# Performance work log

Measured on AMD Instinct MI355X. Metric: run time of the kernel, lower is better.

The kernel has to match this reference:

```python
import jax, jax.numpy as jnp
import numpy as np

# Config (matches init_kwargs)
B, L, D = 2, 2048, 1024
QH, KVH, HD, FFN = 8, 2, 128, 4096
EPS = 1.1920929e-07  # torch RMSNorm default eps = finfo(float32).eps


def _rope_ts():
    d2 = HD // 2
    freq_exp = (2.0 / HD) * jnp.arange(d2, dtype=jnp.float32)
    return 10000.0 ** freq_exp  # [d2]


def _rope(x):
    # x: [B, L, H, HD], rotated in fp32 (matches x.float() in source)
    d2 = HD // 2
    pos = jnp.arange(L, dtype=jnp.float32)
    rad = pos[:, None] / _rope_ts()[None, :]          # [L, d2]
    s = jnp.sin(rad)[None, :, None, :]                # [1, L, 1, d2]
    c = jnp.cos(rad)[None, :, None, :]
    xf = x.astype(jnp.float32)
    x1, x2 = xf[..., :d2], xf[..., d2:]
    return jnp.concatenate([x1 * c - x2 * s, x2 * c + x1 * s], axis=-1).astype(x.dtype)


def _rmsnorm(x, w):
    xf = x.astype(jnp.float32)
    r = jax.lax.rsqrt(jnp.mean(xf * xf, axis=-1, keepdims=True) + EPS)
    return (xf * r).astype(x.dtype) * w


def setup_inputs() -> dict:
    key = jax.random.key(0)
    ks = jax.random.split(key, 9)
    s = 0.02
    return {
        "x": jax.random.normal(ks[0], (B, L, D), dtype=jnp.float32),
        "ln1_w": jnp.ones((D,), dtype=jnp.float32),
        "wq": jax.random.normal(ks[1], (D, QH * HD), dtype=jnp.float32) * s,
        "wk": jax.random.normal(ks[2], (D, KVH * HD), dtype=jnp.float32) * s,
        "wv": jax.random.normal(ks[3], (D, KVH * HD), dtype=jnp.float32) * s,
        "wo": jax.random.normal(ks[4], (QH * HD, D), dtype=jnp.float32) * s,
        "ln2_w": jnp.ones((D,), dtype=jnp.float32),
        "wg": jax.random.normal(ks[5], (D, FFN), dtype=jnp.float32) * s,
        "wu": jax.random.normal(ks[6], (D, FFN), dtype=jnp.float32) * s,
        "wd": jax.random.normal(ks[7], (FFN, D), dtype=jnp.float32) * s,
    }


def reference(x, ln1_w, wq, wk, wv, wo, ln2_w, wg, wu, wd):
    residual = x
    h = _rmsnorm(x, ln1_w)

    q = _rope((h @ wq).reshape(B, L, QH, HD))          # [B,L,QH,HD]
    k = _rope((h @ wk).reshape(B, L, KVH, HD))         # [B,L,KVH,HD]
    v = (h @ wv).reshape(B, L, KVH, HD)

    rep = QH // KVH  # kv_map = floor(arange(QH)*KVH/QH) == repeat each kv head `rep` times
    qh = jnp.transpose(q, (0, 2, 1, 3)).astype(jnp.float32)                       # [B,QH,L,HD]
    kh = jnp.transpose(jnp.repeat(k, rep, axis=2), (0, 2, 1, 3)).astype(jnp.float32)
    vh = jnp.transpose(jnp.repeat(v, rep, axis=2), (0, 2, 1, 3)).astype(jnp.float32)

    scores = jnp.einsum("bhqd,bhkd->bhqk", qh, kh) / jnp.sqrt(jnp.float32(HD))    # [B,QH,L,L]
    causal = jnp.triu(jnp.ones((L, L), dtype=bool), 1)
    scores = jnp.where(causal, -jnp.inf, scores)
    attn = jax.nn.softmax(scores, axis=-1)
    ctx = jnp.einsum("bhqk,bhkd->bhqd", attn, vh)                                 # [B,QH,L,HD]
    ctx = jnp.transpose(ctx, (0, 2, 1, 3)).reshape(B, L, QH * HD).astype(x.dtype)

    x = ctx @ wo + residual
    residual = x
    h = _rmsnorm(x, ln2_w)
    return (jax.nn.silu(h @ wg) * (h @ wu)) @ wd + residual
```

## Files before the change

kernel.cpp:

```cpp
#include <hip/hip_runtime.h>
#include <hip/hip_bf16.h>
#include <math.h>

#define B_ 2
#define L_ 2048
#define D_ 1024
#define QH_ 8
#define KVH_ 2
#define HD_ 128
#define FFN_ 4096
#define T_ (B_ * L_)
#define EPS_ 1.1920929e-07f

typedef __bf16 bf16x8 __attribute__((ext_vector_type(8)));
typedef float floatx4 __attribute__((ext_vector_type(4)));
typedef unsigned short ushortx8 __attribute__((ext_vector_type(8)));

__device__ __forceinline__ unsigned short f2bf(float f) {
  union { float f; unsigned int u; } v;
  v.f = f;
  unsigned int r = v.u + 0x7FFFu + ((v.u >> 16) & 1u);
  return (unsigned short)(r >> 16);
}
__device__ __forceinline__ float bf2f(unsigned short u) {
  union { unsigned int u; float f; } v;
  v.u = ((unsigned int)u) << 16;
  return v.f;
}
__device__ __forceinline__ void gload_lds16(const void* g, void* l) {
  __builtin_amdgcn_global_load_lds((const __attribute__((address_space(1))) void*)g,
                                   (__attribute__((address_space(3))) void*)l, 16, 0, 0);
}

__global__ __launch_bounds__(256) void transpose_cast(const float* __restrict__ in,
                                                      unsigned short* __restrict__ out,
                                                      int K, int N) {
  __shared__ float tile[32][33];
  int n0 = blockIdx.x * 32, k0 = blockIdx.y * 32;
  int tx = threadIdx.x & 31, ty = threadIdx.x >> 5;
  for (int r = ty; r < 32; r += 8) tile[r][tx] = in[(size_t)(k0 + r) * N + n0 + tx];
  __syncthreads();
  for (int r = ty; r < 32; r += 8)
    out[(size_t)(n0 + r) * K + k0 + tx] = f2bf(tile[tx][r]);
}

__global__ __launch_bounds__(256) void rmsnorm_bf16_kernel(const float* __restrict__ x,
                                                           const float* __restrict__ w,
                                                           unsigned short* __restrict__ o) {
  int row = blockIdx.x;
  int t = threadIdx.x;
  const float* xr = x + (size_t)row * D_;
  float4 xv = *(const float4*)(xr + t * 4);
  float ss = xv.x * xv.x + xv.y * xv.y + xv.z * xv.z + xv.w * xv.w;
#pragma unroll
  for (int off = 32; off >= 1; off >>= 1) ss += __shfl_xor(ss, off);
  __shared__ float red[4];
  if ((t & 63) == 0) red[t >> 6] = ss;
  __syncthreads();
  float total = red[0] + red[1] + red[2] + red[3];
  float r = rsqrtf(total * (1.0f / (float)D_) + EPS_);
  float4 wv = *(const float4*)(w + t * 4);
  unsigned short* op = o + (size_t)row * D_ + t * 4;
  op[0] = f2bf(xv.x * r * wv.x);
  op[1] = f2bf(xv.y * r * wv.y);
  op[2] = f2bf(xv.z * r * wv.z);
  op[3] = f2bf(xv.w * r * wv.w);
}

template <int EPI, int MW>
__global__ __launch_bounds__(256) void gemm_bf16(const unsigned short* __restrict__ A,
                                                 const unsigned short* __restrict__ BT,
                                                 const float* __restrict__ R,
                                                 float* __restrict__ C,
                                                 int M, int N, int K) {
  constexpr int AI = MW / 16;
  __shared__ unsigned short As[2 * MW * 32];
  __shared__ unsigned short Bs[128 * 32];
  int t = threadIdx.x;
  int lane = t & 63, wave = t >> 6;
  int m0 = blockIdx.y * (2 * MW), n0 = blockIdx.x * 128;

  int row_a = t >> 2, kc = (t & 3) * 8;
  const unsigned short* ga0 = A + (size_t)(m0 + row_a) * K + kc;
  const unsigned short* ga1 = A + (size_t)(m0 + 64 + row_a) * K + kc;
  const unsigned short* gb0 = BT + (size_t)(n0 + row_a) * K + kc;
  const unsigned short* gb1 = BT + (size_t)(n0 + 64 + row_a) * K + kc;
  unsigned short* lA0 = As + wave * 512;
  unsigned short* lA1 = As + 2048 + wave * 512;
  unsigned short* lB0 = Bs + wave * 512;
  unsigned short* lB1 = Bs + 2048 + wave * 512;

  int wm = (wave & 1) * MW, wn = (wave >> 1) * 64;
  int fr = lane & 15, quad = lane >> 4;
  const unsigned short* arp = As + (size_t)(wm + fr) * 32 + quad * 8;
  const unsigned short* brp = Bs + (size_t)(wn + fr) * 32 + quad * 8;

  floatx4 acc[AI][4];
#pragma unroll
  for (int i = 0; i < AI; i++)
#pragma unroll
    for (int j = 0; j < 4; j++) acc[i][j] = (floatx4){0.f, 0.f, 0.f, 0.f};

  for (int k0 = 0; k0 < K; k0 += 32) {
    gload_lds16(ga0 + k0, lA0);
    if (MW == 64) gload_lds16(ga1 + k0, lA1);
    gload_lds16(gb0 + k0, lB0);
    gload_lds16(gb1 + k0, lB1);
    __syncthreads();
    bf16x8 af[AI], bfr[4];
#pragma unroll
    for (int i = 0; i < AI; i++)
      af[i] = __builtin_bit_cast(bf16x8, *(const ushortx8*)(arp + i * 16 * 32));
#pragma unroll
    for (int j = 0; j < 4; j++)
      bfr[j] = __builtin_bit_cast(bf16x8, *(const ushortx8*)(brp + j * 16 * 32));
#pragma unroll
    for (int i = 0; i < AI; i++)
#pragma unroll
      for (int j = 0; j < 4; j++)
        acc[i][j] = __builtin_amdgcn_mfma_f32_16x16x32_bf16(af[i], bfr[j], acc[i][j], 0, 0, 0);
    __syncthreads();
  }

  int orow = m0 + wm + quad * 4;
  int ocol = n0 + wn + fr;
#pragma unroll
  for (int i = 0; i < AI; i++) {
#pragma unroll
    for (int r = 0; r < 4; r++) {
      int row = orow + i * 16 + r;
#pragma unroll
      for (int j = 0; j < 4; j++) {
        size_t idx = (size_t)row * N + ocol + j * 16;
        float v = acc[i][j][r];
        if (EPI == 0) C[idx] = v;
        else C[idx] = v + R[idx];
      }
    }
  }
}

__global__ __launch_bounds__(256, 2) void gemm_gateup(const unsigned short* __restrict__ A,
                                                      const unsigned short* __restrict__ BgT,
                                                      const unsigned short* __restrict__ BuT,
                                                      unsigned short* __restrict__ Cb,
                                                      int M, int K) {
  constexpr int N = FFN_;
  __shared__ unsigned short As[128 * 32];
  __shared__ unsigned short Bgs[128 * 32];
  __shared__ unsigned short Bus[128 * 32];
  int t = threadIdx.x;
  int lane = t & 63, wave = t >> 6;
  int m0 = blockIdx.y * 128, n0 = blockIdx.x * 128;

  int row_a = t >> 2, kc = (t & 3) * 8;
  const unsigned short* ga0 = A + (size_t)(m0 + row_a) * K + kc;
  const unsigned short* ga1 = A + (size_t)(m0 + 64 + row_a) * K + kc;
  const unsigned short* gg0 = BgT + (size_t)(n0 + row_a) * K + kc;
  const unsigned short* gg1 = BgT + (size_t)(n0 + 64 + row_a) * K + kc;
  const unsigned short* gu0 = BuT + (size_t)(n0 + row_a) * K + kc;
  const unsigned short* gu1 = BuT + (size_t)(n0 + 64 + row_a) * K + kc;
  unsigned short* lA0 = As + wave * 512;
  unsigned short* lA1 = As + 2048 + wave * 512;
  unsigned short* lG0 = Bgs + wave * 512;
  unsigned short* lG1 = Bgs + 2048 + wave * 512;
  unsigned short* lU0 = Bus + wave * 512;
  unsigned short* lU1 = Bus + 2048 + wave * 512;

  int wm = (wave & 1) * 64, wn = (wave >> 1) * 64;
  int fr = lane & 15, quad = lane >> 4;
  const unsigned short* arp = As + (size_t)(wm + fr) * 32 + quad * 8;
  const unsigned short* grp = Bgs + (size_t)(wn + fr) * 32 + quad * 8;
  const unsigned short* urp = Bus + (size_t)(wn + fr) * 32 + quad * 8;

  floatx4 accg[4][4], accu[4][4];
#pragma unroll
  for (int i = 0; i < 4; i++)
#pragma unroll
    for (int j = 0; j < 4; j++) {
      accg[i][j] = (floatx4){0.f, 0.f, 0.f, 0.f};
      accu[i][j] = (floatx4){0.f, 0.f, 0.f, 0.f};
    }

  for (int k0 = 0; k0 < K; k0 += 32) {
    gload_lds16(ga0 + k0, lA0);
    gload_lds16(ga1 + k0, lA1);
    gload_lds16(gg0 + k0, lG0);
    gload_lds16(gg1 + k0, lG1);
    gload_lds16(gu0 + k0, lU0);
    gload_lds16(gu1 + k0, lU1);
    __syncthreads();
    bf16x8 af[4], bg[4], bu[4];
#pragma unroll
    for (int i = 0; i < 4; i++) {
      af[i] = __builtin_bit_cast(bf16x8, *(const ushortx8*)(arp + i * 16 * 32));
      bg[i] = __builtin_bit_cast(bf16x8, *(const ushortx8*)(grp + i * 16 * 32));
      bu[i] = __builtin_bit_cast(bf16x8, *(const ushortx8*)(urp + i * 16 * 32));
    }
#pragma unroll
    for (int i = 0; i < 4; i++)
#pragma unroll
      for (int j = 0; j < 4; j++) {
        accg[i][j] = __builtin_amdgcn_mfma_f32_16x16x32_bf16(af[i], bg[j], accg[i][j], 0, 0, 0);
        accu[i][j] = __builtin_amdgcn_mfma_f32_16x16x32_bf16(af[i], bu[j], accu[i][j], 0, 0, 0);
      }
    __syncthreads();
  }

  int orow = m0 + wm + quad * 4;
  int ocol = n0 + wn + fr;
#pragma unroll
  for (int i = 0; i < 4; i++) {
#pragma unroll
    for (int r = 0; r < 4; r++) {
      int row = orow + i * 16 + r;
#pragma unroll
      for (int j = 0; j < 4; j++) {
        float g = accg[i][j][r];
        float u = accu[i][j][r];
        Cb[(size_t)row * N + ocol + j * 16] = f2bf(g / (1.f + __expf(-g)) * u);
      }
    }
  }
}

__global__ __launch_bounds__(256) void rope_kernel(float* __restrict__ x, int stride,
                                                   int nh_shift, int total) {
  int idx = blockIdx.x * 256 + threadIdx.x;
  if (idx >= total) return;
  int d2 = idx & 63;
  int rest = idx >> 6;
  int NH = 1 << nh_shift;
  int head = rest & (NH - 1);
  int tok = rest >> nh_shift;
  int pos = tok & (L_ - 1);
  float inv_ts = expf(-0.14391156831f * (float)d2);
  float rad = (float)pos * inv_ts;
  float s = sinf(rad), c = cosf(rad);
  float* p = x + (size_t)tok * stride + head * HD_ + d2;
  float x1 = p[0], x2 = p[64];
  p[0] = x1 * c - x2 * s;
  p[64] = x2 * c + x1 * s;
}

__global__ __launch_bounds__(256) void convert_k_rope(const float* __restrict__ qkv,
                                                      unsigned short* __restrict__ Kb) {
  int id = blockIdx.x * 256 + threadIdx.x;
  int d2 = id & 63;
  int key = (id >> 6) & (L_ - 1);
  int kvh = (id >> 17) & 1;
  int b = id >> 18;
  const float* src = qkv + (size_t)(b * L_ + key) * 1536 + 1024 + kvh * HD_ + d2;
  float x1 = src[0], x2 = src[64];
  float inv_ts = expf(-0.14391156831f * (float)d2);
  float rad = (float)key * inv_ts;
  float s = sinf(rad), c = cosf(rad);
  unsigned short* dst = Kb + ((size_t)(b * KVH_ + kvh) * L_ + key) * HD_;
  int sw = key & 15;
  dst[((d2 >> 3) ^ sw) * 8 + (d2 & 7)] = f2bf(x1 * c - x2 * s);
  dst[(((d2 >> 3) | 8) ^ sw) * 8 + (d2 & 7)] = f2bf(x2 * c + x1 * s);
}

__global__ __launch_bounds__(256) void convert_v(const float* __restrict__ qkv,
                                                 unsigned short* __restrict__ Vt) {
  __shared__ float tile[32][66];
  int key0 = blockIdx.x * 64, hd0 = blockIdx.y * 32;
  int bk = blockIdx.z;
  int b = bk >> 1, kvh = bk & 1;
  int t = threadIdx.x;
  int key_l = t >> 2, hq = t & 3;
  const float* src =
      qkv + (size_t)(b * L_ + key0 + key_l) * 1536 + 1280 + kvh * HD_ + hd0 + hq * 8;
  float4 v0 = *(const float4*)src;
  float4 v1 = *(const float4*)(src + 4);
  tile[hq * 8 + 0][key_l] = v0.x;
  tile[hq * 8 + 1][key_l] = v0.y;
  tile[hq * 8 + 2][key_l] = v0.z;
  tile[hq * 8 + 3][key_l] = v0.w;
  tile[hq * 8 + 4][key_l] = v1.x;
  tile[hq * 8 + 5][key_l] = v1.y;
  tile[hq * 8 + 6][key_l] = v1.z;
  tile[hq * 8 + 7][key_l] = v1.w;
  __syncthreads();
  int hdl = t >> 3, cp = t & 7;
  int kc = cp ^ (hdl & 7);
  ushortx8 ob;
#pragma unroll
  for (int j = 0; j < 8; j++) ob[j] = f2bf(tile[hdl][kc * 8 + j]);
  unsigned short* dst = Vt + ((size_t)bk * HD_ + hd0 + hdl) * L_ + key0 + cp * 8;
  *(ushortx8*)dst = ob;
}

__global__ __launch_bounds__(256) void attn_mfma(const float* __restrict__ qkv,
                                                 const unsigned short* __restrict__ Kb,
                                                 const unsigned short* __restrict__ Vt,
                                                 unsigned short* __restrict__ ctx) {
  __shared__ unsigned short Ks[64 * 128];
  __shared__ unsigned short Vs[128 * 64];
  __shared__ unsigned short Ps[4][16 * 72];
  const float scale = 0.08838834764831843f;
  int id = blockIdx.x;
  int bh = id & 15;
  int p_ = id >> 4;
  int qt = (p_ < 16) ? p_ : 47 - p_;
  int b = bh >> 3, h = bh & 7;
  int bk = b * KVH_ + (h >> 2);
  int q0 = qt * 64;
  int t = threadIdx.x, lane = t & 63, w = t >> 6;
  int fr = lane & 15, quad = lane >> 4;

  const float* qrow = qkv + (size_t)(b * L_ + q0 + w * 16 + fr) * 1536 + h * HD_;
  bf16x8 qf[4];
#pragma unroll
  for (int kb = 0; kb < 4; kb++) {
    float4 a = *(const float4*)(qrow + kb * 32 + quad * 8);
    float4 c = *(const float4*)(qrow + kb * 32 + quad * 8 + 4);
    qf[kb][0] = (__bf16)(a.x * scale);
    qf[kb][1] = (__bf16)(a.y * scale);
    qf[kb][2] = (__bf16)(a.z * scale);
    qf[kb][3] = (__bf16)(a.w * scale);
    qf[kb][4] = (__bf16)(c.x * scale);
    qf[kb][5] = (__bf16)(c.y * scale);
    qf[kb][6] = (__bf16)(c.z * scale);
    qf[kb][7] = (__bf16)(c.w * scale);
  }

  floatx4 o_acc[8];
#pragma unroll
  for (int nt = 0; nt < 8; nt++) o_acc[nt] = (floatx4){0.f, 0.f, 0.f, 0.f};
  float m_r[4], l_r[4];
#pragma unroll
  for (int r = 0; r < 4; r++) {
    m_r[r] = -__builtin_inff();
    l_r[r] = 0.f;
  }
  unsigned short* Psw = Ps[w];
  const unsigned short* kgb = Kb + (size_t)bk * L_ * HD_;
  const unsigned short* vgb = Vt + (size_t)bk * HD_ * L_;
  int rowg0 = q0 + w * 16 + quad * 4;

  for (int kt = 0; kt <= qt; kt++) {
    int kstart = kt * 64;
    __syncthreads();
    const unsigned short* ksrc = kgb + (size_t)kstart * HD_;
#pragma unroll
    for (int it = 0; it < 4; it++) {
      int sl = it * 4 + w;
      gload_lds16(ksrc + sl * 512 + lane * 8, Ks + sl * 512);
    }
#pragma unroll
    for (int it = 0; it < 4; it++) {
      int sl = it * 4 + w;
      gload_lds16(vgb + (size_t)(sl * 8 + (lane >> 3)) * L_ + kstart + (lane & 7) * 8,
                  Vs + sl * 512);
    }
    __syncthreads();

    floatx4 s_acc[4];
#pragma unroll
    for (int jt = 0; jt < 4; jt++) s_acc[jt] = (floatx4){0.f, 0.f, 0.f, 0.f};
#pragma unroll
    for (int kb = 0; kb < 4; kb++) {
#pragma unroll
      for (int jt = 0; jt < 4; jt++) {
        bf16x8 kf = __builtin_bit_cast(
            bf16x8, *(const ushortx8*)(Ks + (jt * 16 + fr) * 128 +
                                       (((kb * 4 + quad) ^ fr) * 8)));
        s_acc[jt] = __builtin_amdgcn_mfma_f32_16x16x32_bf16(qf[kb], kf, s_acc[jt], 0, 0, 0);
      }
    }

    float pvv[4][4];
    float alpha[4];
#pragma unroll
    for (int r = 0; r < 4; r++) {
      float mt = -__builtin_inff();
#pragma unroll
      for (int jt = 0; jt < 4; jt++) {
        int keyg = kstart + jt * 16 + fr;
        float sv = (keyg <= rowg0 + r) ? s_acc[jt][r] : -__builtin_inff();
        pvv[jt][r] = sv;
        mt = fmaxf(mt, sv);
      }
      mt = fmaxf(mt, __shfl_xor(mt, 1));
      mt = fmaxf(mt, __shfl_xor(mt, 2));
      mt = fmaxf(mt, __shfl_xor(mt, 4));
      mt = fmaxf(mt, __shfl_xor(mt, 8));
      float mn = fmaxf(m_r[r], mt);
      alpha[r] = __expf(m_r[r] - mn);
      m_r[r] = mn;
      float lt = 0.f;
#pragma unroll
      for (int jt = 0; jt < 4; jt++) {
        float pp = __expf(pvv[jt][r] - mn);
        pvv[jt][r] = pp;
        lt += pp;
      }
      lt += __shfl_xor(lt, 1);
      lt += __shfl_xor(lt, 2);
      lt += __shfl_xor(lt, 4);
      lt += __shfl_xor(lt, 8);
      l_r[r] = l_r[r] * alpha[r] + lt;
    }
#pragma unroll
    for (int nt = 0; nt < 8; nt++) {
      o_acc[nt][0] *= alpha[0];
      o_acc[nt][1] *= alpha[1];
      o_acc[nt][2] *= alpha[2];
      o_acc[nt][3] *= alpha[3];
    }
#pragma unroll
    for (int r = 0; r < 4; r++)
#pragma unroll
      for (int jt = 0; jt < 4; jt++)
        Psw[(quad * 4 + r) * 72 + jt * 16 + fr] = f2bf(pvv[jt][r]);
    bf16x8 pf0 = __builtin_bit_cast(bf16x8, *(const ushortx8*)(Psw + fr * 72 + quad * 8));
    bf16x8 pf1 =
        __builtin_bit_cast(bf16x8, *(const ushortx8*)(Psw + fr * 72 + 32 + quad * 8));
#pragma unroll
    for (int nt = 0; nt < 8; nt++) {
      bf16x8 vf0 = __builtin_bit_cast(
          bf16x8,
          *(const ushortx8*)(Vs + (nt * 16 + fr) * 64 + ((quad ^ (fr & 7)) * 8)));
      bf16x8 vf1 = __builtin_bit_cast(
          bf16x8,
          *(const ushortx8*)(Vs + (nt * 16 + fr) * 64 + (((4 + quad) ^ (fr & 7)) * 8)));
      o_acc[nt] = __builtin_amdgcn_mfma_f32_16x16x32_bf16(pf0, vf0, o_acc[nt], 0, 0, 0);
      o_acc[nt] = __builtin_amdgcn_mfma_f32_16x16x32_bf16(pf1, vf1, o_acc[nt], 0, 0, 0);
    }
  }

  unsigned short* ob =
      ctx + (size_t)(b * L_ + q0 + w * 16 + quad * 4) * 1024 + h * HD_ + fr;
#pragma unroll
  for (int r = 0; r < 4; r++) {
    float inv = 1.f / l_r[r];
    unsigned short* orow = ob + (size_t)r * 1024;
#pragma unroll
    for (int nt = 0; nt < 8; nt++) orow[nt * 16] = f2bf(o_acc[nt][r] * inv);
  }
}

extern "C" void kernel_launch(void* const* d_in, const int* in_sizes, int n_in,
                              void* d_out, int out_size, void* d_ws, size_t ws_size,
                              hipStream_t stream) {
  const float* x    = (const float*)d_in[0];
  const float* ln1w = (const float*)d_in[1];
  const float* wq   = (const float*)d_in[2];
  const float* wk   = (const float*)d_in[3];
  const float* wvp  = (const float*)d_in[4];
  const float* wo   = (const float*)d_in[5];
  const float* ln2w = (const float*)d_in[6];
  const float* wg   = (const float*)d_in[7];
  const float* wu   = (const float*)d_in[8];
  const float* wd   = (const float*)d_in[9];
  float* out = (float*)d_out;
  char* ws = (char*)d_ws;

  unsigned short* wT = (unsigned short*)ws;
  unsigned short* wqkvT = wT;
  unsigned short* woT = wT + 1572864;
  unsigned short* wgT = wT + 2621440;
  unsigned short* wuT = wT + 6815744;
  unsigned short* wdT = wT + 11010048;

  unsigned short* h_bf = (unsigned short*)(ws + 30408704);
  float* qkv = (float*)(ws + 38797312);
  float* x2 = qkv;
  unsigned short* h2_bf = (unsigned short*)(ws + 38797312 + 16777216);
  unsigned short* ctx_bf = h_bf;

  size_t gbase = 63963136;
  bool full = ws_size >= (size_t)97517568;
  unsigned short* Kb = (unsigned short*)(ws + gbase);
  unsigned short* Vt = (unsigned short*)(ws + gbase + 2097152u);
  unsigned short* gu = (unsigned short*)(ws + gbase);

  dim3 blk(256);

  transpose_cast<<<dim3(32, 32), blk, 0, stream>>>(wq, wqkvT, 1024, 1024);
  transpose_cast<<<dim3(8, 32), blk, 0, stream>>>(wk, wqkvT + 1048576, 1024, 256);
  transpose_cast<<<dim3(8, 32), blk, 0, stream>>>(wvp, wqkvT + 1310720, 1024, 256);
  transpose_cast<<<dim3(32, 32), blk, 0, stream>>>(wo, woT, 1024, 1024);
  transpose_cast<<<dim3(128, 32), blk, 0, stream>>>(wg, wgT, 1024, 4096);
  transpose_cast<<<dim3(128, 32), blk, 0, stream>>>(wu, wuT, 1024, 4096);
  transpose_cast<<<dim3(32, 128), blk, 0, stream>>>(wd, wdT, 4096, 1024);

  rmsnorm_bf16_kernel<<<T_, blk, 0, stream>>>(x, ln1w, h_bf);
  gemm_bf16<0, 32><<<dim3(12, 64), blk, 0, stream>>>(h_bf, wqkvT, nullptr, qkv,
                                                     T_, 1536, 1024);
  rope_kernel<<<(T_ * QH_ * 64) / 256, blk, 0, stream>>>(qkv, 1536, 3, T_ * QH_ * 64);
  convert_k_rope<<<(B_ * KVH_ * L_ * 64) / 256, blk, 0, stream>>>(qkv, Kb);
  convert_v<<<dim3(32, 4, 4), blk, 0, stream>>>(qkv, Vt);
  attn_mfma<<<dim3(512), blk, 0, stream>>>(qkv, Kb, Vt, ctx_bf);
  gemm_bf16<1, 32><<<dim3(8, 64), blk, 0, stream>>>(ctx_bf, woT, x, x2, T_, 1024, 1024);
  rmsnorm_bf16_kernel<<<T_, blk, 0, stream>>>(x2, ln2w, h2_bf);

  if (full) {
    gemm_gateup<<<dim3(32, 32), blk, 0, stream>>>(h2_bf, wgT, wuT, gu, T_, 1024);
    gemm_bf16<1, 32><<<dim3(8, 64), blk, 0, stream>>>(gu, wdT, x2, out, T_, 1024, FFN_);
  } else {
    for (int c = 0; c < 4; c++) {
      const unsigned short* h2c = h2_bf + (size_t)c * 1024 * 1024;
      const float* x2c = x2 + (size_t)c * 1024 * 1024;
      float* outc = out + (size_t)c * 1024 * 1024;
      gemm_gateup<<<dim3(32, 8), blk, 0, stream>>>(h2c, wgT, wuT, gu, 1024, 1024);
      gemm_bf16<1, 32><<<dim3(8, 16), blk, 0, stream>>>(gu, wdT, x2c, outc, 1024, 1024, FFN_);
    }
  }
}
```

Before: 426.7 us.

## Fuse weight prep with rmsnorm, store QKV as bf16, fuse RoPE into attention

```diff
diff --git a/kernel.cpp b/kernel.cpp
--- a/kernel.cpp
+++ b/kernel.cpp
@@ -15,6 +15,7 @@
 typedef __bf16 bf16x8 __attribute__((ext_vector_type(8)));
 typedef float floatx4 __attribute__((ext_vector_type(4)));
 typedef unsigned short ushortx8 __attribute__((ext_vector_type(8)));
+typedef unsigned short ushortx4 __attribute__((ext_vector_type(4)));
 
 __device__ __forceinline__ unsigned short f2bf(float f) {
   union { float f; unsigned int u; } v;
@@ -32,29 +33,31 @@
                                    (__attribute__((address_space(3))) void*)l, 16, 0, 0);
 }
 
-__global__ __launch_bounds__(256) void transpose_cast(const float* __restrict__ in,
-                                                      unsigned short* __restrict__ out,
-                                                      int K, int N) {
+__device__ __forceinline__ void tile_tc(const float* __restrict__ in,
+                                        unsigned short* __restrict__ out,
+                                        int K, int N, int n0, int k0) {
   __shared__ float tile[32][33];
-  int n0 = blockIdx.x * 32, k0 = blockIdx.y * 32;
-  int tx = threadIdx.x & 31, ty = threadIdx.x >> 5;
+  int t = threadIdx.x;
+  int tx = t & 31, ty = t >> 5;
   for (int r = ty; r < 32; r += 8) tile[r][tx] = in[(size_t)(k0 + r) * N + n0 + tx];
   __syncthreads();
-  for (int r = ty; r < 32; r += 8)
-    out[(size_t)(n0 + r) * K + k0 + tx] = f2bf(tile[tx][r]);
-}
-
-__global__ __launch_bounds__(256) void rmsnorm_bf16_kernel(const float* __restrict__ x,
-                                                           const float* __restrict__ w,
-                                                           unsigned short* __restrict__ o) {
-  int row = blockIdx.x;
+  int nr = t >> 3, kq = t & 7;
+  ushortx4 o4;
+#pragma unroll
+  for (int j = 0; j < 4; j++) o4[j] = f2bf(tile[kq * 4 + j][nr]);
+  *(ushortx4*)(out + (size_t)(n0 + nr) * K + k0 + kq * 4) = o4;
+}
+
+__device__ __forceinline__ void rmsnorm_row(const float* __restrict__ x,
+                                            const float* __restrict__ w,
+                                            unsigned short* __restrict__ o, int row) {
+  __shared__ float red[4];
   int t = threadIdx.x;
   const float* xr = x + (size_t)row * D_;
   float4 xv = *(const float4*)(xr + t * 4);
   float ss = xv.x * xv.x + xv.y * xv.y + xv.z * xv.z + xv.w * xv.w;
 #pragma unroll
   for (int off = 32; off >= 1; off >>= 1) ss += __shfl_xor(ss, off);
-  __shared__ float red[4];
   if ((t & 63) == 0) red[t >> 6] = ss;
   __syncthreads();
   float total = red[0] + red[1] + red[2] + red[3];
@@ -67,11 +70,44 @@
   op[3] = f2bf(xv.w * r * wv.w);
 }
 
+__global__ __launch_bounds__(256) void prep_all(
+    const float* __restrict__ wq, const float* __restrict__ wk,
+    const float* __restrict__ wv, const float* __restrict__ wo,
+    const float* __restrict__ wg, const float* __restrict__ wu,
+    const float* __restrict__ wd, unsigned short* __restrict__ wT,
+    const float* __restrict__ x, const float* __restrict__ ln1w,
+    unsigned short* __restrict__ h_bf) {
+  int bid = blockIdx.x;
+  if (bid < 14848) {
+    const float* in;
+    unsigned short* out;
+    int K, N, nt, base;
+    if (bid < 1024)       { in = wq; out = wT;            K = 1024; N = 1024; nt = 32;  base = 0; }
+    else if (bid < 1280)  { in = wk; out = wT + 1048576;  K = 1024; N = 256;  nt = 8;   base = 1024; }
+    else if (bid < 1536)  { in = wv; out = wT + 1310720;  K = 1024; N = 256;  nt = 8;   base = 1280; }
+    else if (bid < 2560)  { in = wo; out = wT + 1572864;  K = 1024; N = 1024; nt = 32;  base = 1536; }
+    else if (bid < 6656)  { in = wg; out = wT + 2621440;  K = 1024; N = 4096; nt = 128; base = 2560; }
+    else if (bid < 10752) { in = wu; out = wT + 6815744;  K = 1024; N = 4096; nt = 128; base = 6656; }
+    else                  { in = wd; out = wT + 11010048; K = 4096; N = 1024; nt = 32;  base = 10752; }
+    int idx = bid - base;
+    tile_tc(in, out, K, N, (idx % nt) * 32, (idx / nt) * 32);
+  } else {
+    rmsnorm_row(x, ln1w, h_bf, bid - 14848);
+  }
+}
+
+__global__ __launch_bounds__(256) void rmsnorm_bf16_kernel(const float* __restrict__ x,
+                                                           const float* __restrict__ w,
+                                                           unsigned short* __restrict__ o) {
+  rmsnorm_row(x, w, o, blockIdx.x);
+}
+
 template <int EPI, int MW>
 __global__ __launch_bounds__(256) void gemm_bf16(const unsigned short* __restrict__ A,
                                                  const unsigned short* __restrict__ BT,
                                                  const float* __restrict__ R,
                                                  float* __restrict__ C,
+                                                 unsigned short* __restrict__ Cb,
                                                  int M, int N, int K) {
   constexpr int AI = MW / 16;
   __shared__ unsigned short As[2 * MW * 32];
@@ -134,7 +170,9 @@
         size_t idx = (size_t)row * N + ocol + j * 16;
         float v = acc[i][j][r];
         if (EPI == 0) C[idx] = v;
-        else C[idx] = v + R[idx];
+        else if (EPI == 1) C[idx] = v + R[idx];
+        else if (EPI == 2) C[idx] = v + C[idx];
+        else Cb[idx] = f2bf(v);
       }
     }
   }
@@ -224,74 +262,50 @@
   }
 }
 
-__global__ __launch_bounds__(256) void rope_kernel(float* __restrict__ x, int stride,
-                                                   int nh_shift, int total) {
-  int idx = blockIdx.x * 256 + threadIdx.x;
-  if (idx >= total) return;
-  int d2 = idx & 63;
-  int rest = idx >> 6;
-  int NH = 1 << nh_shift;
-  int head = rest & (NH - 1);
-  int tok = rest >> nh_shift;
-  int pos = tok & (L_ - 1);
-  float inv_ts = expf(-0.14391156831f * (float)d2);
-  float rad = (float)pos * inv_ts;
-  float s = sinf(rad), c = cosf(rad);
-  float* p = x + (size_t)tok * stride + head * HD_ + d2;
-  float x1 = p[0], x2 = p[64];
-  p[0] = x1 * c - x2 * s;
-  p[64] = x2 * c + x1 * s;
-}
-
-__global__ __launch_bounds__(256) void convert_k_rope(const float* __restrict__ qkv,
-                                                      unsigned short* __restrict__ Kb) {
-  int id = blockIdx.x * 256 + threadIdx.x;
-  int d2 = id & 63;
-  int key = (id >> 6) & (L_ - 1);
-  int kvh = (id >> 17) & 1;
-  int b = id >> 18;
-  const float* src = qkv + (size_t)(b * L_ + key) * 1536 + 1024 + kvh * HD_ + d2;
-  float x1 = src[0], x2 = src[64];
-  float inv_ts = expf(-0.14391156831f * (float)d2);
-  float rad = (float)key * inv_ts;
-  float s = sinf(rad), c = cosf(rad);
-  unsigned short* dst = Kb + ((size_t)(b * KVH_ + kvh) * L_ + key) * HD_;
-  int sw = key & 15;
-  dst[((d2 >> 3) ^ sw) * 8 + (d2 & 7)] = f2bf(x1 * c - x2 * s);
-  dst[(((d2 >> 3) | 8) ^ sw) * 8 + (d2 & 7)] = f2bf(x2 * c + x1 * s);
-}
-
-__global__ __launch_bounds__(256) void convert_v(const float* __restrict__ qkv,
-                                                 unsigned short* __restrict__ Vt) {
-  __shared__ float tile[32][66];
-  int key0 = blockIdx.x * 64, hd0 = blockIdx.y * 32;
-  int bk = blockIdx.z;
-  int b = bk >> 1, kvh = bk & 1;
-  int t = threadIdx.x;
-  int key_l = t >> 2, hq = t & 3;
-  const float* src =
-      qkv + (size_t)(b * L_ + key0 + key_l) * 1536 + 1280 + kvh * HD_ + hd0 + hq * 8;
-  float4 v0 = *(const float4*)src;
-  float4 v1 = *(const float4*)(src + 4);
-  tile[hq * 8 + 0][key_l] = v0.x;
-  tile[hq * 8 + 1][key_l] = v0.y;
-  tile[hq * 8 + 2][key_l] = v0.z;
-  tile[hq * 8 + 3][key_l] = v0.w;
-  tile[hq * 8 + 4][key_l] = v1.x;
-  tile[hq * 8 + 5][key_l] = v1.y;
-  tile[hq * 8 + 6][key_l] = v1.z;
-  tile[hq * 8 + 7][key_l] = v1.w;
-  __syncthreads();
-  int hdl = t >> 3, cp = t & 7;
-  int kc = cp ^ (hdl & 7);
-  ushortx8 ob;
-#pragma unroll
-  for (int j = 0; j < 8; j++) ob[j] = f2bf(tile[hdl][kc * 8 + j]);
-  unsigned short* dst = Vt + ((size_t)bk * HD_ + hd0 + hdl) * L_ + key0 + cp * 8;
-  *(ushortx8*)dst = ob;
-}
-
-__global__ __launch_bounds__(256) void attn_mfma(const float* __restrict__ qkv,
+__global__ __launch_bounds__(256) void convert_kv(const unsigned short* __restrict__ qkvb,
+                                                  unsigned short* __restrict__ Kb,
+                                                  unsigned short* __restrict__ Vt) {
+  __shared__ unsigned short tile_s[32][72];
+  int bid = blockIdx.x;
+  if (bid < 2048) {
+    int id = bid * 256 + threadIdx.x;
+    int d2 = id & 63;
+    int key = (id >> 6) & (L_ - 1);
+    int kvh = (id >> 17) & 1;
+    int b = id >> 18;
+    const unsigned short* src =
+        qkvb + (size_t)(b * L_ + key) * 1536 + 1024 + kvh * HD_ + d2;
+    float x1 = bf2f(src[0]), x2 = bf2f(src[64]);
+    float inv_ts = expf(-0.14391156831f * (float)d2);
+    float rad = (float)key * inv_ts;
+    float s = sinf(rad), c = cosf(rad);
+    unsigned short* dst = Kb + ((size_t)(b * KVH_ + kvh) * L_ + key) * HD_;
+    int sw = key & 15;
+    dst[((d2 >> 3) ^ sw) * 8 + (d2 & 7)] = f2bf(x1 * c - x2 * s);
+    dst[(((d2 >> 3) | 8) ^ sw) * 8 + (d2 & 7)] = f2bf(x2 * c + x1 * s);
+  } else {
+    int id = bid - 2048;
+    int keyt = id & 31, hdt = (id >> 5) & 3, bk = id >> 7;
+    int key0 = keyt * 64, hd0 = hdt * 32;
+    int b = bk >> 1, kvh = bk & 1;
+    int t = threadIdx.x;
+    int key_l = t >> 2, hq = t & 3;
+    const unsigned short* src = qkvb + (size_t)(b * L_ + key0 + key_l) * 1536 + 1280 +
+                                kvh * HD_ + hd0 + hq * 8;
+    ushortx8 v8 = *(const ushortx8*)src;
+#pragma unroll
+    for (int j = 0; j < 8; j++) tile_s[hq * 8 + j][key_l] = v8[j];
+    __syncthreads();
+    int hdl = t >> 3, cp = t & 7;
+    int kc = cp ^ (hdl & 7);
+    ushortx8 ob;
+#pragma unroll
+    for (int j = 0; j < 8; j++) ob[j] = tile_s[hdl][kc * 8 + j];
+    *(ushortx8*)(Vt + ((size_t)bk * HD_ + hd0 + hdl) * L_ + key0 + cp * 8) = ob;
+  }
+}
+
+__global__ __launch_bounds__(256) void attn_mfma(const unsigned short* __restrict__ qkvb,
                                                  const unsigned short* __restrict__ Kb,
                                                  const unsigned short* __restrict__ Vt,
                                                  unsigned short* __restrict__ ctx) {
@@ -309,20 +323,28 @@
   int t = threadIdx.x, lane = t & 63, w = t >> 6;
   int fr = lane & 15, quad = lane >> 4;
 
-  const float* qrow = qkv + (size_t)(b * L_ + q0 + w * 16 + fr) * 1536 + h * HD_;
+  int pos = q0 + w * 16 + fr;
+  const unsigned short* qrow = qkvb + (size_t)(b * L_ + pos) * 1536 + h * HD_;
+  float q32[4][8];
+#pragma unroll
+  for (int kb = 0; kb < 4; kb++) {
+    ushortx8 u = *(const ushortx8*)(qrow + kb * 32 + quad * 8);
+#pragma unroll
+    for (int j = 0; j < 8; j++) q32[kb][j] = bf2f(u[j]);
+  }
   bf16x8 qf[4];
 #pragma unroll
-  for (int kb = 0; kb < 4; kb++) {
-    float4 a = *(const float4*)(qrow + kb * 32 + quad * 8);
-    float4 c = *(const float4*)(qrow + kb * 32 + quad * 8 + 4);
-    qf[kb][0] = (__bf16)(a.x * scale);
-    qf[kb][1] = (__bf16)(a.y * scale);
-    qf[kb][2] = (__bf16)(a.z * scale);
-    qf[kb][3] = (__bf16)(a.w * scale);
-    qf[kb][4] = (__bf16)(c.x * scale);
-    qf[kb][5] = (__bf16)(c.y * scale);
-    qf[kb][6] = (__bf16)(c.z * scale);
-    qf[kb][7] = (__bf16)(c.w * scale);
+  for (int kb2 = 0; kb2 < 2; kb2++) {
+#pragma unroll
+    for (int j = 0; j < 8; j++) {
+      int d2 = kb2 * 32 + quad * 8 + j;
+      float inv_ts = expf(-0.14391156831f * (float)d2);
+      float rad = (float)pos * inv_ts;
+      float s = sinf(rad), c = cosf(rad);
+      float x1 = q32[kb2][j], x2 = q32[kb2 + 2][j];
+      qf[kb2][j] = (__bf16)((x1 * c - x2 * s) * scale);
+      qf[kb2 + 2][j] = (__bf16)((x2 * c + x1 * s) * scale);
+    }
   }
 
   floatx4 o_acc[8];
@@ -463,49 +485,25 @@
   unsigned short* wgT = wT + 2621440;
   unsigned short* wuT = wT + 6815744;
   unsigned short* wdT = wT + 11010048;
-
   unsigned short* h_bf = (unsigned short*)(ws + 30408704);
-  float* qkv = (float*)(ws + 38797312);
-  float* x2 = qkv;
-  unsigned short* h2_bf = (unsigned short*)(ws + 38797312 + 16777216);
+  unsigned short* qkvb = (unsigned short*)(ws + 38797312);
+  unsigned short* h2_bf = (unsigned short*)(ws + 51380224);
+  unsigned short* Kb = (unsigned short*)(ws + 59768832);
+  unsigned short* Vt = (unsigned short*)(ws + 61865984);
+  unsigned short* gu = (unsigned short*)(ws + 59768832);
   unsigned short* ctx_bf = h_bf;
 
-  size_t gbase = 63963136;
-  bool full = ws_size >= (size_t)97517568;
-  unsigned short* Kb = (unsigned short*)(ws + gbase);
-  unsigned short* Vt = (unsigned short*)(ws + gbase + 2097152u);
-  unsigned short* gu = (unsigned short*)(ws + gbase);
-
   dim3 blk(256);
 
-  transpose_cast<<<dim3(32, 32), blk, 0, stream>>>(wq, wqkvT, 1024, 1024);
-  transpose_cast<<<dim3(8, 32), blk, 0, stream>>>(wk, wqkvT + 1048576, 1024, 256);
-  transpose_cast<<<dim3(8, 32), blk, 0, stream>>>(wvp, wqkvT + 1310720, 1024, 256);
-  transpose_cast<<<dim3(32, 32), blk, 0, stream>>>(wo, woT, 1024, 1024);
-  transpose_cast<<<dim3(128, 32), blk, 0, stream>>>(wg, wgT, 1024, 4096);
-  transpose_cast<<<dim3(128, 32), blk, 0, stream>>>(wu, wuT, 1024, 4096);
-  transpose_cast<<<dim3(32, 128), blk, 0, stream>>>(wd, wdT, 4096, 1024);
-
-  rmsnorm_bf16_kernel<<<T_, blk, 0, stream>>>(x, ln1w, h_bf);
-  gemm_bf16<0, 32><<<dim3(12, 64), blk, 0, stream>>>(h_bf, wqkvT, nullptr, qkv,
-                                                     T_, 1536, 1024);
-  rope_kernel<<<(T_ * QH_ * 64) / 256, blk, 0, stream>>>(qkv, 1536, 3, T_ * QH_ * 64);
-  convert_k_rope<<<(B_ * KVH_ * L_ * 64) / 256, blk, 0, stream>>>(qkv, Kb);
-  convert_v<<<dim3(32, 4, 4), blk, 0, stream>>>(qkv, Vt);
-  attn_mfma<<<dim3(512), blk, 0, stream>>>(qkv, Kb, Vt, ctx_bf);
-  gemm_bf16<1, 32><<<dim3(8, 64), blk, 0, stream>>>(ctx_bf, woT, x, x2, T_, 1024, 1024);
-  rmsnorm_bf16_kernel<<<T_, blk, 0, stream>>>(x2, ln2w, h2_bf);
-
-  if (full) {
-    gemm_gateup<<<dim3(32, 32), blk, 0, stream>>>(h2_bf, wgT, wuT, gu, T_, 1024);
-    gemm_bf16<1, 32><<<dim3(8, 64), blk, 0, stream>>>(gu, wdT, x2, out, T_, 1024, FFN_);
-  } else {
-    for (int c = 0; c < 4; c++) {
-      const unsigned short* h2c = h2_bf + (size_t)c * 1024 * 1024;
-      const float* x2c = x2 + (size_t)c * 1024 * 1024;
-      float* outc = out + (size_t)c * 1024 * 1024;
-      gemm_gateup<<<dim3(32, 8), blk, 0, stream>>>(h2c, wgT, wuT, gu, 1024, 1024);
-      gemm_bf16<1, 32><<<dim3(8, 16), blk, 0, stream>>>(gu, wdT, x2c, outc, 1024, 1024, FFN_);
-    }
-  }
-}
+  prep_all<<<14848 + T_, blk, 0, stream>>>(wq, wk, wvp, wo, wg, wu, wd, wT, x, ln1w, h_bf);
+  gemm_bf16<3, 32><<<dim3(12, 64), blk, 0, stream>>>(h_bf, wqkvT, nullptr, nullptr,
+                                                     qkvb, T_, 1536, 1024);
+  convert_kv<<<2560, blk, 0, stream>>>(qkvb, Kb, Vt);
+  attn_mfma<<<512, blk, 0, stream>>>(qkvb, Kb, Vt, ctx_bf);
+  gemm_bf16<1, 32><<<dim3(8, 64), blk, 0, stream>>>(ctx_bf, woT, x, out, nullptr,
+                                                    T_, 1024, 1024);
+  rmsnorm_bf16_kernel<<<T_, blk, 0, stream>>>(out, ln2w, h2_bf);
+  gemm_gateup<<<dim3(32, 32), blk, 0, stream>>>(h2_bf, wgT, wuT, gu, T_, 1024);
+  gemm_bf16<2, 32><<<dim3(8, 64), blk, 0, stream>>>(gu, wdT, nullptr, out, nullptr,
+                                                    T_, 1024, FFN_);
+}
```

After: 413.7 us. -3.1%, faster.
